# Performance work log

Measured on AMD Instinct MI355X. Metric: run time of the kernel, lower is better.

Reference implementation:

```python
import jax, jax.numpy as jnp
import numpy as np

LRELU_SLOPE = 0.2
LN_EPS = 1e-5
BAND_EPS = 1e-8


def setup_inputs() -> dict:
    key = jax.random.key(0)
    ks = jax.random.split(key, 3)
    B, C, H, W = 32, 3, 1024, 1024
    num_bands, feat_dim = 16, 256
    fin = C * num_bands * 3  # 144
    x = jax.random.normal(ks[0], (B, C, H, W), dtype=jnp.float32)
    W1 = jax.random.normal(ks[1], (fin, feat_dim), dtype=jnp.float32) * 0.05
    b1 = jnp.zeros((feat_dim,), jnp.float32)
    W2 = jax.random.normal(ks[2], (feat_dim, feat_dim), dtype=jnp.float32) * 0.05
    b2 = jnp.zeros((feat_dim,), jnp.float32)
    gamma = jnp.ones((feat_dim,), jnp.float32)
    beta = jnp.zeros((feat_dim,), jnp.float32)
    return {"x": x, "W1": W1, "b1": b1, "W2": W2, "b2": b2, "gamma": gamma, "beta": beta}


def reference(x, W1, b1, W2, b2, gamma, beta):
    B, C, H, W = x.shape
    nb = W1.shape[0] // (C * 3)  # num_bands
    # --- FFT magnitude ---
    mag = jnp.abs(jnp.fft.rfft2(x, norm='ortho'))  # [B,C,H,Wr]
    Wr = mag.shape[-1]
    # --- radial bin index (exact same >= comparisons as the torch band loop) ---
    u = jnp.fft.rfftfreq(W).astype(mag.dtype)          # [Wr]
    v = jnp.fft.fftfreq(H).astype(mag.dtype)           # [H]
    radius = jnp.sqrt(u[None, :] ** 2 + v[:, None] ** 2)  # [H,Wr]
    max_r = radius.max()
    lowers = max_r * jnp.arange(nb + 1, dtype=mag.dtype) / nb  # i=0..nb
    # bin = (#thresholds <= radius) - 1 ; radius==max_r lands in segment nb (excluded)
    bins = jnp.sum(radius[..., None] >= lowers[None, None, :], axis=-1) - 1  # [H,Wr]
    seg = bins.reshape(-1).astype(jnp.int32)  # [H*Wr]
    K = nb + 1
    # --- single-pass segmented reductions over all pixels ---
    magf = mag.reshape(B * C, -1).T                      # [HWr, B*C]
    counts = jax.ops.segment_sum(jnp.ones(seg.shape, mag.dtype), seg, num_segments=K)  # [K]
    s1 = jax.ops.segment_sum(magf, seg, num_segments=K)             # [K, BC]
    s2 = jax.ops.segment_sum(magf * magf, seg, num_segments=K)      # [K, BC]
    mx = jax.ops.segment_max(magf, seg, num_segments=K)             # [K, BC]
    denom = counts[:, None] + BAND_EPS
    mean = s1 / denom
    # sum over band of (mag-mean)^2 = s2 - 2*mean*s1 + count*mean^2
    var = (s2 - 2.0 * mean * s1 + counts[:, None] * mean * mean) / denom
    # drop segment nb (radius == max_r is excluded by `radius < upper`), then sqrt
    mean = mean[:nb]
    var = jnp.maximum(var[:nb], 0.0)
    std = jnp.sqrt(var)
    # torch max is over mag*mask (zeros elsewhere) -> floor at 0
    mx = jnp.maximum(mx[:nb], 0.0)
    # --- assemble [B, nb*3*C] in band-major, (mean,max,std), channel order ---
    def to_bkc(a):
        return a.reshape(nb, B, C).transpose(1, 0, 2)  # [B, nb, C]
    feat_vec = jnp.stack([to_bkc(mean), to_bkc(mx), to_bkc(std)], axis=2)  # [B, nb, 3, C]
    feat_vec = feat_vec.reshape(B, nb * 3 * C)
    # --- MLP: Linear -> LeakyReLU(0.2) -> Linear -> LayerNorm ---
    h = feat_vec @ W1 + b1
    h = jnp.where(h >= 0, h, LRELU_SLOPE * h)
    h = h @ W2 + b2
    mu = jnp.mean(h, axis=-1, keepdims=True)
    va = jnp.mean((h - mu) ** 2, axis=-1, keepdims=True)
    return (h - mu) / jnp.sqrt(va + LN_EPS) * gamma + beta
```

## Files before the change

### kernel.cpp

```cpp
#include <hip/hip_runtime.h>
#include <hip/hip_fp16.h>
#include <math.h>

#define HH    1024
#define WWID  1024
#define WR    513
#define NIMG  96
#define NGRP  65
#define KSEG  17
#define FEAT  256
#define FIN   144

__device__ __forceinline__ float2 cmul(float2 a, float2 b) {
    return make_float2(a.x * b.x - a.y * b.y, a.x * b.y + a.y * b.x);
}

__device__ __forceinline__ int radial_bin(int hf, int k) {
    const float maxr = 0.707106781186547524f;
    float v = (float)(hf < 512 ? hf : hf - 1024) * (1.0f / 1024.0f);
    float u = (float)k * (1.0f / 1024.0f);
    float rad = sqrtf(u * u + v * v);
    int bin = 0;
#pragma unroll
    for (int l = 1; l <= 16; ++l) {
        float lower = (maxr * (float)l) * 0.0625f;
        bin += (rad >= lower) ? 1 : 0;
    }
    return bin;
}

__device__ __forceinline__ int fast_bin(float rad) {
    int c = (int)(rad * 22.62741699796952f);
    if (c > 16) c = 16;
    if (c < 16 && rad >= (0.707106781186547524f * (float)(c + 1)) * 0.0625f) c++;
    else if (rad < (0.707106781186547524f * (float)c) * 0.0625f) c--;
    return c;
}

__device__ __forceinline__ float2 wave_fft_AB(float2 a[16], int l) {
    constexpr float TW16C[8] = {1.f, 0.9238795325112867f, 0.7071067811865476f,
                                0.3826834323650898f, 0.f, -0.3826834323650898f,
                                -0.7071067811865476f, -0.9238795325112867f};
    constexpr float TW16S[8] = {0.f, -0.3826834323650898f, -0.7071067811865476f,
                                -0.9238795325112867f, -1.f, -0.9238795325112867f,
                                -0.7071067811865476f, -0.3826834323650898f};
#pragma unroll
    for (int m = 2; m <= 16; m <<= 1) {
        const int half = m >> 1;
        const int tstep = 16 / m;
#pragma unroll
        for (int bse = 0; bse < 16; bse += m) {
#pragma unroll
            for (int jj = 0; jj < 8; ++jj) {
                if (jj < half) {
                    float2 w = make_float2(TW16C[jj * tstep], TW16S[jj * tstep]);
                    float2 tv = cmul(a[bse + half + jj], w);
                    float2 u0 = a[bse + jj];
                    a[bse + jj]        = make_float2(u0.x + tv.x, u0.y + tv.y);
                    a[bse + half + jj] = make_float2(u0.x - tv.x, u0.y - tv.y);
                }
            }
        }
    }
    float sn, cs;
    sincosf((float)l * (-6.28318530717958647692f / 1024.0f), &sn, &cs);
    float2 w1 = make_float2(cs, sn);
    float2 w2 = cmul(w1, w1);
    float2 w3 = cmul(w2, w1);
    float2 w4 = cmul(w2, w2);
    float2 w8 = cmul(w4, w4);
    float2 w12 = cmul(w8, w4);
    a[1] = cmul(a[1], w1);
    a[2] = cmul(a[2], w2);
    a[3] = cmul(a[3], w3);
#pragma unroll
    for (int r = 4; r < 16; ++r) {
        float2 hi = (r >> 2) == 1 ? w4 : ((r >> 2) == 2 ? w8 : w12);
        float2 p = cmul(a[r], hi);
        int lo = r & 3;
        if (lo == 1) p = cmul(p, w1);
        else if (lo == 2) p = cmul(p, w2);
        else if (lo == 3) p = cmul(p, w3);
        a[r] = p;
    }
    return cmul(w8, w8);
}

__device__ __forceinline__ void wave_fft_C(float2 a[16], int l, float2 u) {
#pragma unroll
    for (int half = 32; half >= 1; half >>= 1) {
        const bool up = (l & half) != 0;
        const float sgn = up ? -1.0f : 1.0f;
        const float twx = up ? -u.x : 1.0f;
        const float twy = up ? -u.y : 0.0f;
#pragma unroll
        for (int r = 0; r < 16; ++r) {
            float ox = __shfl_xor(a[r].x, half);
            float oy = __shfl_xor(a[r].y, half);
            float sx = fmaf(sgn, a[r].x, ox);
            float sy = fmaf(sgn, a[r].y, oy);
            a[r].x = fmaf(sx, twx, -(sy * twy));
            a[r].y = fmaf(sx, twy, sy * twx);
        }
        if (half > 1) u = cmul(u, u);
    }
}

static __device__ __constant__ int BR4[16] = {0,8,4,12,2,10,6,14,1,9,5,13,3,11,7,15};

__global__ __launch_bounds__(512) void k_rowfft(const float* __restrict__ x,
                                                __half2* __restrict__ interm,
                                                int img0) {
    __shared__ __half2 tile[WR][17];
    const int t = threadIdx.x;
    const int w = t >> 6;
    const int l = t & 63;
    const int blk = blockIdx.x;
    const int iy = blockIdx.y;
    const int img = img0 + iy;
    const int h1 = blk + 128 * w;
    const int h2 = h1 + 64;

    const float* r1 = x + ((size_t)img * HH + h1) * WWID;
    const float* r2 = x + ((size_t)img * HH + h2) * WWID;
    float2 a[16];
#pragma unroll
    for (int j = 0; j < 16; ++j) {
        int i = l + 64 * j;
        a[BR4[j]] = make_float2(r1[i], r2[i]);
    }

    float2 u16 = wave_fft_AB(a, l);
    wave_fft_C(a, l, u16);

    const int b = (int)(__brev((unsigned)l) >> 26);
#pragma unroll
    for (int r = 0; r < 16; ++r) {
        float2 znr;
        if (r == 0) {
            int cblk = (64 - b) & 63;
            int q = (int)(__brev((unsigned)cblk) >> 26);
            znr.x = __shfl(a[0].x, q);
            znr.y = __shfl(a[0].y, q);
        } else {
            znr.x = __shfl_xor(a[16 - r].x, 63);
            znr.y = __shfl_xor(a[16 - r].y, 63);
        }
        int k = 16 * b + r;
        if (k <= 512) {
            int cc = b & 15;
            tile[k][(2 * w) ^ cc] =
                __floats2half2_rn(0.5f * (a[r].x + znr.x), 0.5f * (a[r].y - znr.y));
            tile[k][(2 * w + 1) ^ cc] =
                __floats2half2_rn(0.5f * (a[r].y + znr.y), 0.5f * (znr.x - a[r].x));
        }
    }
    __syncthreads();

    __half2* gout = interm + (size_t)iy * WR * 1024 + blk * 16;
    for (int idx = t; idx < WR * 16; idx += 512) {
        int k = idx >> 4;
        int r = idx & 15;
        gout[(size_t)k * 1024 + r] = tile[k][r ^ ((k >> 4) & 15)];
    }
}

__global__ __launch_bounds__(512) void k_colfft(const __half2* __restrict__ interm,
                                                float* __restrict__ partials,
                                                int img0) {
    __shared__ float wsum[8][KSEG][2];
    __shared__ unsigned wmax[8][KSEG];
    const int t = threadIdx.x;
    const int g = blockIdx.x;
    const int iy = blockIdx.y;
    const int img = img0 + iy;
    const int wv = t >> 6;
    const int l = t & 63;
    const int k = g * 8 + wv;

    for (int i = t; i < 8 * KSEG; i += 512) {
        int w = i / KSEG, bb = i - w * KSEG;
        wsum[w][bb][0] = 0.f; wsum[w][bb][1] = 0.f; wmax[w][bb] = 0u;
    }
    __syncthreads();

    if (k <= 512) {
        const uint4* gq = (const uint4*)(interm + ((size_t)iy * WR + k) * 1024 + l * 16);
        union QU { uint4 q[4]; __half2 h[16]; } qu;
        qu.q[0] = gq[0]; qu.q[1] = gq[1]; qu.q[2] = gq[2]; qu.q[3] = gq[3];
        float2 a[16];
#pragma unroll
        for (int j = 0; j < 16; ++j)
            a[BR4[j]] = __half22float2(qu.h[j]);

        float2 u16 = wave_fft_AB(a, l);
        wave_fft_C(a, l, u16);

        const int b = (int)(__brev((unsigned)l) >> 26);
        const int h0 = 16 * b;
        const float uf = (float)k * (1.0f / 1024.0f);
        const float uu = uf * uf;
        float vf0 = (float)(h0 < 512 ? h0 : h0 - 1024) * (1.0f / 1024.0f);
        float vfF = (float)(h0 + 15 < 512 ? h0 + 15 : h0 + 15 - 1024) * (1.0f / 1024.0f);
        int binF = fast_bin(sqrtf(fmaf(vf0, vf0, uu)));
        int binL = fast_bin(sqrtf(fmaf(vfF, vfF, uu)));
        const int bHi = (binF > binL) ? binF : binL;
        const float Lmid = (0.707106781186547524f * (float)bHi) * 0.0625f;
        const float Lmid2 = Lmid * Lmid;

        float sA1 = 0.f, sA2 = 0.f, mA = 0.f;
        float sB1 = 0.f, sB2 = 0.f, mB = 0.f;
#pragma unroll
        for (int r = 0; r < 16; ++r) {
            int h = h0 + r;
            float vf = (float)(h < 512 ? h : h - 1024) * (1.0f / 1024.0f);
            float s = fmaf(vf, vf, uu);
            float2 z = a[r];
            float p2 = fmaf(z.x, z.x, z.y * z.y);
            float m = sqrtf(p2) * (1.0f / 1024.0f);
            float msq = p2 * (1.0f / 1048576.0f);
            bool c = (s >= Lmid2);
            sA1 += c ? m : 0.f;
            sA2 += c ? msq : 0.f;
            mA = fmaxf(mA, c ? m : 0.f);
            sB1 += c ? 0.f : m;
            sB2 += c ? 0.f : msq;
            mB = fmaxf(mB, c ? 0.f : m);
        }

        atomicAdd(&wsum[wv][bHi][0], sA1);
        atomicAdd(&wsum[wv][bHi][1], sA2);
        atomicMax(&wmax[wv][bHi], __float_as_uint(mA));
        if (bHi > 0) {
            atomicAdd(&wsum[wv][bHi - 1][0], sB1);
            atomicAdd(&wsum[wv][bHi - 1][1], sB2);
            atomicMax(&wmax[wv][bHi - 1], __float_as_uint(mB));
        }
    }
    __syncthreads();

    if (t < KSEG) {
        float aS = 0.f, bS = 0.f, cM = 0.f;
#pragma unroll
        for (int w = 0; w < 8; ++w) {
            aS += wsum[w][t][0];
            bS += wsum[w][t][1];
            cM = fmaxf(cM, __uint_as_float(wmax[w][t]));
        }
        float* dstp = partials + ((size_t)img * NGRP + g) * (KSEG * 3) + t * 3;
        dstp[0] = aS; dstp[1] = bS; dstp[2] = cM;
    }
}

__global__ __launch_bounds__(256) void k_counts(unsigned* __restrict__ counts) {
    int cnt[KSEG];
#pragma unroll
    for (int l = 0; l < KSEG; ++l) cnt[l] = 0;
    const int total = HH * WR;
    for (int idx = blockIdx.x * 256 + threadIdx.x; idx < total; idx += gridDim.x * 256) {
        int h = idx / WR;
        int k = idx - h * WR;
        int bin = radial_bin(h, k);
#pragma unroll
        for (int l = 0; l < KSEG; ++l) cnt[l] += (bin == l) ? 1 : 0;
    }
    const int lane = threadIdx.x & 63;
#pragma unroll
    for (int l = 0; l < KSEG; ++l) {
        int c = cnt[l];
        for (int off = 32; off > 0; off >>= 1) c += __shfl_xor(c, off);
        if (lane == 0 && c > 0) atomicAdd(&counts[l], (unsigned)c);
    }
}

__global__ __launch_bounds__(256) void k_mlp(const float* __restrict__ partials,
                                             const unsigned* __restrict__ counts,
                                             const float* __restrict__ W1,
                                             const float* __restrict__ b1,
                                             const float* __restrict__ W2,
                                             const float* __restrict__ b2,
                                             const float* __restrict__ gamma,
                                             const float* __restrict__ beta,
                                             float* __restrict__ out) {
    __shared__ float feat[FIN];
    __shared__ float h1s[FEAT];
    __shared__ float red[FEAT];
    const int b = blockIdx.x;
    const int t = threadIdx.x;
    if (t < 48) {
        int c = t / 16;
        int bin = t % 16;
        const float* p = partials + ((size_t)(b * 3 + c) * NGRP) * (KSEG * 3) + bin * 3;
        float s1 = 0.f, s2 = 0.f, mxv = 0.f;
        for (int gg = 0; gg < NGRP; ++gg) {
            s1 += p[gg * (KSEG * 3) + 0];
            s2 += p[gg * (KSEG * 3) + 1];
            mxv = fmaxf(mxv, p[gg * (KSEG * 3) + 2]);
        }
        float cntf = (float)counts[bin];
        float denom = cntf + 1e-8f;
        float mean = s1 / denom;
        float var = (s2 - 2.0f * mean * s1 + cntf * mean * mean) / denom;
        var = fmaxf(var, 0.0f);
        float sd = sqrtf(var);
        mxv = fmaxf(mxv, 0.0f);
        feat[bin * 9 + 0 + c] = mean;
        feat[bin * 9 + 3 + c] = mxv;
        feat[bin * 9 + 6 + c] = sd;
    }
    __syncthreads();

    float acc = b1[t];
    for (int i = 0; i < FIN; ++i) acc += feat[i] * W1[i * FEAT + t];
    acc = (acc >= 0.0f) ? acc : 0.2f * acc;
    h1s[t] = acc;
    __syncthreads();

    float acc2 = b2[t];
    for (int i = 0; i < FEAT; ++i) acc2 += h1s[i] * W2[i * FEAT + t];

    red[t] = acc2;
    __syncthreads();
    for (int off = 128; off > 0; off >>= 1) {
        if (t < off) red[t] += red[t + off];
        __syncthreads();
    }
    float mu = red[0] * (1.0f / 256.0f);
    __syncthreads();
    float dvt = acc2 - mu;
    red[t] = dvt * dvt;
    __syncthreads();
    for (int off = 128; off > 0; off >>= 1) {
        if (t < off) red[t] += red[t + off];
        __syncthreads();
    }
    float va = red[0] * (1.0f / 256.0f);
    out[(size_t)b * FEAT + t] = dvt / sqrtf(va + 1e-5f) * gamma[t] + beta[t];
}

extern "C" void kernel_launch(void* const* d_in, const int* in_sizes, int n_in,
                              void* d_out, int out_size, void* d_ws, size_t ws_size,
                              hipStream_t stream) {
    const float* x     = (const float*)d_in[0];
    const float* W1    = (const float*)d_in[1];
    const float* b1    = (const float*)d_in[2];
    const float* W2    = (const float*)d_in[3];
    const float* b2    = (const float*)d_in[4];
    const float* gamma = (const float*)d_in[5];
    const float* beta  = (const float*)d_in[6];
    float* out = (float*)d_out;

    char* ws = (char*)d_ws;
    unsigned* counts = (unsigned*)ws;
    float* partials = (float*)(ws + 256);
    const size_t partialsBytes = (size_t)NIMG * NGRP * KSEG * 3 * sizeof(float);
    const size_t intermOff = (256 + partialsBytes + 255) & ~(size_t)255;
    __half2* interm = (__half2*)(ws + intermOff);
    const size_t perImg = (size_t)WR * 1024 * sizeof(__half2);

    long long avail = (long long)ws_size - (long long)intermOff;
    int chunk = (avail > 0) ? (int)(avail / (long long)perImg) : 0;
    if (chunk > NIMG) chunk = NIMG;
    if (chunk < 1) chunk = 1;

    hipMemsetAsync(counts, 0, KSEG * sizeof(unsigned), stream);
    k_counts<<<dim3(128), dim3(256), 0, stream>>>(counts);

    for (int img0 = 0; img0 < NIMG; img0 += chunk) {
        int n = NIMG - img0;
        if (n > chunk) n = chunk;
        k_rowfft<<<dim3(64, n), dim3(512), 0, stream>>>(x, interm, img0);
        k_colfft<<<dim3(NGRP, n), dim3(512), 0, stream>>>(interm, partials, img0);
    }

    k_mlp<<<dim3(32), dim3(256), 0, stream>>>(partials, counts, W1, b1, W2, b2,
                                              gamma, beta, out);
}
```

Measured before the change: 466.4 us.

## Move two-for-one real FFT split from row pass into column pass

The row FFT now stores the raw packed complex spectrum of each row pair (1024 bins × 512 packed entries) without doing the Hermitian even/odd separation. The column kernel loads the bin k together with its mirror bin 1024−k and performs the split while unpacking, so the shuffles disappear from the row kernel. The row kernel also moves to 1024-thread blocks with a new row pairing (h, h+512), and twiddle generation switches to the fast __sinf/__cosf intrinsics. In exchange, the column kernel issues two scattered loads per lane instead of one contiguous load, the intermediate buffer shape changes, and the fast intrinsics lose some accuracy.

```diff
diff --git a/kernel.cpp b/kernel.cpp
--- a/kernel.cpp
+++ b/kernel.cpp
@@ -62,9 +62,8 @@
             }
         }
     }
-    float sn, cs;
-    sincosf((float)l * (-6.28318530717958647692f / 1024.0f), &sn, &cs);
-    float2 w1 = make_float2(cs, sn);
+    float ang = (float)l * (-6.28318530717958647692f / 1024.0f);
+    float2 w1 = make_float2(__cosf(ang), __sinf(ang));
     float2 w2 = cmul(w1, w1);
     float2 w3 = cmul(w2, w1);
     float2 w4 = cmul(w2, w2);
@@ -108,21 +107,21 @@
 
 static __device__ __constant__ int BR4[16] = {0,8,4,12,2,10,6,14,1,9,5,13,3,11,7,15};
 
-__global__ __launch_bounds__(512) void k_rowfft(const float* __restrict__ x,
-                                                __half2* __restrict__ interm,
-                                                int img0) {
-    __shared__ __half2 tile[WR][17];
+__global__ __launch_bounds__(1024) void k_rowfft(const float* __restrict__ x,
+                                                 __half2* __restrict__ interm,
+                                                 int img0) {
+    __shared__ __half2 tile[1024][17];
     const int t = threadIdx.x;
     const int w = t >> 6;
     const int l = t & 63;
     const int blk = blockIdx.x;
     const int iy = blockIdx.y;
     const int img = img0 + iy;
-    const int h1 = blk + 128 * w;
-    const int h2 = h1 + 64;
-
-    const float* r1 = x + ((size_t)img * HH + h1) * WWID;
-    const float* r2 = x + ((size_t)img * HH + h2) * WWID;
+    const int hA = ((w & 7) << 6) + 2 * blk + (w >> 3);
+    const int hB = hA + 512;
+
+    const float* r1 = x + ((size_t)img * HH + hA) * WWID;
+    const float* r2 = x + ((size_t)img * HH + hB) * WWID;
     float2 a[16];
 #pragma unroll
     for (int j = 0; j < 16; ++j) {
@@ -136,32 +135,18 @@
     const int b = (int)(__brev((unsigned)l) >> 26);
 #pragma unroll
     for (int r = 0; r < 16; ++r) {
-        float2 znr;
-        if (r == 0) {
-            int cblk = (64 - b) & 63;
-            int q = (int)(__brev((unsigned)cblk) >> 26);
-            znr.x = __shfl(a[0].x, q);
-            znr.y = __shfl(a[0].y, q);
-        } else {
-            znr.x = __shfl_xor(a[16 - r].x, 63);
-            znr.y = __shfl_xor(a[16 - r].y, 63);
-        }
         int k = 16 * b + r;
-        if (k <= 512) {
-            int cc = b & 15;
-            tile[k][(2 * w) ^ cc] =
-                __floats2half2_rn(0.5f * (a[r].x + znr.x), 0.5f * (a[r].y - znr.y));
-            tile[k][(2 * w + 1) ^ cc] =
-                __floats2half2_rn(0.5f * (a[r].y + znr.y), 0.5f * (znr.x - a[r].x));
-        }
-    }
-    __syncthreads();
-
-    __half2* gout = interm + (size_t)iy * WR * 1024 + blk * 16;
-    for (int idx = t; idx < WR * 16; idx += 512) {
+        tile[k][w ^ (b & 15)] = __floats2half2_rn(a[r].x, a[r].y);
+    }
+    __syncthreads();
+
+    __half2* gout = interm + (size_t)iy * 1024 * 512 + blk * 16;
+#pragma unroll
+    for (int it = 0; it < 16; ++it) {
+        int idx = t + it * 1024;
         int k = idx >> 4;
-        int r = idx & 15;
-        gout[(size_t)k * 1024 + r] = tile[k][r ^ ((k >> 4) & 15)];
+        int s = idx & 15;
+        gout[(size_t)k * 512 + s] = tile[k][s ^ ((k >> 4) & 15)];
     }
 }
 
@@ -185,13 +170,21 @@
     __syncthreads();
 
     if (k <= 512) {
-        const uint4* gq = (const uint4*)(interm + ((size_t)iy * WR + k) * 1024 + l * 16);
-        union QU { uint4 q[4]; __half2 h[16]; } qu;
-        qu.q[0] = gq[0]; qu.q[1] = gq[1]; qu.q[2] = gq[2]; qu.q[3] = gq[3];
+        const int kn = (1024 - k) & 1023;
+        const uint4* ps = (const uint4*)(interm + ((size_t)iy * 1024 + k) * 512 + l * 8);
+        const uint4* pn = (const uint4*)(interm + ((size_t)iy * 1024 + kn) * 512 + l * 8);
+        union QU { uint4 q[2]; __half2 h[8]; } us, un;
+        us.q[0] = ps[0]; us.q[1] = ps[1];
+        un.q[0] = pn[0]; un.q[1] = pn[1];
+
         float2 a[16];
 #pragma unroll
-        for (int j = 0; j < 16; ++j)
-            a[BR4[j]] = __half22float2(qu.h[j]);
+        for (int m = 0; m < 8; ++m) {
+            float2 zs = __half22float2(us.h[m]);
+            float2 zn = __half22float2(un.h[m]);
+            a[BR4[m]]     = make_float2(0.5f * (zs.x + zn.x), 0.5f * (zs.y - zn.y));
+            a[BR4[m + 8]] = make_float2(0.5f * (zs.y + zn.y), 0.5f * (zn.x - zs.x));
+        }
 
         float2 u16 = wave_fft_AB(a, l);
         wave_fft_C(a, l, u16);
@@ -356,7 +349,7 @@
     const size_t partialsBytes = (size_t)NIMG * NGRP * KSEG * 3 * sizeof(float);
     const size_t intermOff = (256 + partialsBytes + 255) & ~(size_t)255;
     __half2* interm = (__half2*)(ws + intermOff);
-    const size_t perImg = (size_t)WR * 1024 * sizeof(__half2);
+    const size_t perImg = (size_t)1024 * 512 * sizeof(__half2);
 
     long long avail = (long long)ws_size - (long long)intermOff;
     int chunk = (avail > 0) ? (int)(avail / (long long)perImg) : 0;
@@ -369,7 +362,7 @@
     for (int img0 = 0; img0 < NIMG; img0 += chunk) {
         int n = NIMG - img0;
         if (n > chunk) n = chunk;
-        k_rowfft<<<dim3(64, n), dim3(512), 0, stream>>>(x, interm, img0);
+        k_rowfft<<<dim3(32, n), dim3(1024), 0, stream>>>(x, interm, img0);
         k_colfft<<<dim3(NGRP, n), dim3(512), 0, stream>>>(interm, partials, img0);
     }
 
```

New measurement: 447.0 us. 1.04x faster.
